# Performance work log

Hardware: AMD Instinct MI355X
Metric: run time of the kernel (lower is better)

## Reference

```python
import jax, jax.numpy as jnp
import numpy as np

C = 128          # channel_size
H = 2            # num_head
HD = C // H      # per-head dim = 64
SCALE = C ** 0.5 # note: module scales by sqrt(channel_size), not sqrt(head_dim)


def setup_inputs() -> dict:
    key = jax.random.key(0)
    k_x, k_w, k_b = jax.random.split(key, 3)
    x = jax.random.normal(k_x, (8, 64, 256, C), dtype=jnp.float32)
    # nn.Linear(C, 3C): weight [3C, C], bias [3C]; y = x @ W.T + b
    bound = 1.0 / np.sqrt(C)
    W_qkv = jax.random.uniform(k_w, (3 * C, C), dtype=jnp.float32, minval=-bound, maxval=bound)
    b_qkv = jax.random.uniform(k_b, (3 * C,), dtype=jnp.float32, minval=-bound, maxval=bound)
    return {"x": x, "W_qkv": W_qkv, "b_qkv": b_qkv}


def reference(x, W_qkv, b_qkv):
    b, l, g, _ = x.shape
    qkv = jnp.einsum('blgc,dc->blgd', x, W_qkv) + b_qkv        # [b,l,g,3C]
    # rearrange 'b l g (d h c) -> d b l h g c'
    qkv = qkv.reshape(b, l, g, 3, H, HD)
    qkv = jnp.transpose(qkv, (3, 0, 1, 4, 2, 5))               # [3,b,l,h,g,c]
    q, k, v = qkv[0], qkv[1], qkv[2]
    score = jnp.einsum('blhgc,blhkc->blhgk', q, k) / SCALE      # [b,l,h,g,g]
    score = jax.nn.softmax(score, axis=-1)
    out = jnp.einsum('blhgk,blhkc->blhgc', score, v)            # [b,l,h,g,c]
    # rearrange 'b l h g c -> b l g (h c)'
    out = jnp.transpose(out, (0, 1, 3, 2, 4)).reshape(b, l, g, H * HD)
    return out
```

## Files before the change

kernel.cpp:

```cpp
#include <hip/hip_runtime.h>
#include <hip/hip_bf16.h>


typedef __bf16 bf16x8 __attribute__((ext_vector_type(8)));
typedef float  f32x4  __attribute__((ext_vector_type(4)));
typedef float  f32x16 __attribute__((ext_vector_type(16)));

#define MFMA16(a, b, c) __builtin_amdgcn_mfma_f32_16x16x32_bf16((a), (b), (c), 0, 0, 0)
#define MFMA32(a, b, c) __builtin_amdgcn_mfma_f32_32x32x16_bf16((a), (b), (c), 0, 0, 0)

namespace dmsa {

constexpr int G  = 256;
constexpr int C  = 128;
constexpr int HD = 64;
constexpr float QSCALE = 1.4426950408889634f * 0.08838834764831845f;

__device__ __forceinline__ unsigned pack2(float a, float b) {
    union { __hip_bfloat162 h; unsigned u; } c;
    c.h = __float22bfloat162_rn(make_float2(a, b));
    return c.u;
}
__device__ __forceinline__ uint2 pack4(float a, float b, float c, float d) {
    uint2 r; r.x = pack2(a, b); r.y = pack2(c, d); return r;
}
__device__ __forceinline__ uint4 pack8(const float* p) {
    uint4 r;
    r.x = pack2(p[0], p[1]); r.y = pack2(p[2], p[3]);
    r.z = pack2(p[4], p[5]); r.w = pack2(p[6], p[7]);
    return r;
}
__device__ __forceinline__ bf16x8 lds8(const ushort* p) { return *(const bf16x8*)p; }
__device__ __forceinline__ bf16x8 ldg8(const ushort* p) { return *(const bf16x8*)p; }
__device__ __forceinline__ bf16x8 ld8f(const float* __restrict__ p) {
    float t[8];
    *(float4*)t       = *(const float4*)p;
    *(float4*)(t + 4) = *(const float4*)(p + 4);
    union { uint4 u; bf16x8 v; } c;
    c.u = pack8(t);
    return c.v;
}

__global__ void convw(const float* __restrict__ W, ushort* __restrict__ wbf) {
    int t = blockIdx.x * 256 + threadIdx.x;
    float tmp[8];
    const float* p = W + (size_t)t * 8;
    *(float4*)tmp       = *(const float4*)p;
    *(float4*)(tmp + 4) = *(const float4*)(p + 4);
    *(uint4*)(wbf + (size_t)t * 8) = pack8(tmp);
}

__global__ __launch_bounds__(512, 4)
void fused(const float* __restrict__ x, const ushort* __restrict__ wb,
           const float* __restrict__ bias, float* __restrict__ out)
{
    __shared__ ushort kc[G * 72];
    __shared__ ushort vc[HD * 264];

    const int tid = threadIdx.x, wv = tid >> 6, lane = tid & 63;
    const int l16 = lane & 15, quad = lane >> 4;
    const int l32 = lane & 31, hl = lane >> 5;

    const int b  = blockIdx.x;
    const int L  = ((b & 7) << 7) | (b >> 3);
    const int bl = L >> 1, h = L & 1;

    const float*  xr = x  + (size_t)bl * G * C;
    const ushort* Wq = wb + (size_t)(h * HD) * C;
    const ushort* Wk = wb + (size_t)(C + h * HD) * C;
    const ushort* Wv = wb + (size_t)(2 * C + h * HD) * C;

    const int r0 = wv * 32;
    const f32x4 z4 = {0.f, 0.f, 0.f, 0.f};

    bf16x8 xf[2][4];
    #pragma unroll
    for (int i = 0; i < 2; ++i)
        #pragma unroll
        for (int kk = 0; kk < 4; ++kk)
            xf[i][kk] = ld8f(xr + (size_t)(r0 + i * 16 + l16) * C + kk * 32 + quad * 8);

    f32x4 qacc[4][2];
    #pragma unroll
    for (int mi = 0; mi < 4; ++mi)
        #pragma unroll
        for (int ni = 0; ni < 2; ++ni) qacc[mi][ni] = z4;
    #pragma unroll
    for (int kk = 0; kk < 4; ++kk)
        #pragma unroll
        for (int mi = 0; mi < 4; ++mi) {
            bf16x8 a = ldg8(Wq + (size_t)(mi * 16 + l16) * C + kk * 32 + quad * 8);
            #pragma unroll
            for (int ni = 0; ni < 2; ++ni)
                qacc[mi][ni] = MFMA16(a, xf[ni][kk], qacc[mi][ni]);
        }
    ushort* qs = kc + r0 * 72;
    #pragma unroll
    for (int mi = 0; mi < 4; ++mi) {
        float4 bs = *(const float4*)(bias + h * HD + mi * 16 + quad * 4);
        #pragma unroll
        for (int ni = 0; ni < 2; ++ni)
            *(uint2*)(qs + (ni * 16 + l16) * 72 + mi * 16 + quad * 4) =
                pack4((qacc[mi][ni][0] + bs.x) * QSCALE,
                      (qacc[mi][ni][1] + bs.y) * QSCALE,
                      (qacc[mi][ni][2] + bs.z) * QSCALE,
                      (qacc[mi][ni][3] + bs.w) * QSCALE);
    }
    bf16x8 qf[4];
    #pragma unroll
    for (int kk = 0; kk < 4; ++kk)
        qf[kk] = lds8(qs + l32 * 72 + kk * 16 + hl * 8);

    {
        f32x4 kacc[4][2];
        #pragma unroll
        for (int mi = 0; mi < 4; ++mi)
            #pragma unroll
            for (int nt = 0; nt < 2; ++nt) kacc[mi][nt] = z4;
        #pragma unroll
        for (int kk = 0; kk < 4; ++kk)
            #pragma unroll
            for (int mi = 0; mi < 4; ++mi) {
                bf16x8 a = ldg8(Wk + (size_t)(mi * 16 + l16) * C + kk * 32 + quad * 8);
                #pragma unroll
                for (int nt = 0; nt < 2; ++nt)
                    kacc[mi][nt] = MFMA16(a, xf[nt][kk], kacc[mi][nt]);
            }
        #pragma unroll
        for (int mi = 0; mi < 4; ++mi) {
            float4 bs = *(const float4*)(bias + C + h * HD + mi * 16 + quad * 4);
            #pragma unroll
            for (int nt = 0; nt < 2; ++nt)
                *(uint2*)(kc + (r0 + nt * 16 + l16) * 72 + mi * 16 + quad * 4) =
                    pack4(kacc[mi][nt][0] + bs.x, kacc[mi][nt][1] + bs.y,
                          kacc[mi][nt][2] + bs.z, kacc[mi][nt][3] + bs.w);
        }
    }

    {
        f32x4 vacc[2][4];
        #pragma unroll
        for (int mt = 0; mt < 2; ++mt)
            #pragma unroll
            for (int nt = 0; nt < 4; ++nt) vacc[mt][nt] = z4;
        #pragma unroll
        for (int kk = 0; kk < 4; ++kk)
            #pragma unroll
            for (int nt = 0; nt < 4; ++nt) {
                bf16x8 bw = ldg8(Wv + (size_t)(nt * 16 + l16) * C + kk * 32 + quad * 8);
                #pragma unroll
                for (int mt = 0; mt < 2; ++mt)
                    vacc[mt][nt] = MFMA16(xf[mt][kk], bw, vacc[mt][nt]);
            }
        #pragma unroll
        for (int nt = 0; nt < 4; ++nt) {
            float bv = bias[2 * C + h * HD + nt * 16 + l16];
            #pragma unroll
            for (int mt = 0; mt < 2; ++mt)
                *(uint2*)(vc + (nt * 16 + l16) * 264 + r0 + mt * 16 + quad * 4) =
                    pack4(vacc[mt][nt][0] + bv, vacc[mt][nt][1] + bv,
                          vacc[mt][nt][2] + bv, vacc[mt][nt][3] + bv);
        }
    }

    __syncthreads();

    float lacc = 0.f;
    f32x16 oacc[2];
    #pragma unroll
    for (int mt = 0; mt < 2; ++mt)
        #pragma unroll
        for (int r = 0; r < 16; ++r) oacc[mt][r] = 0.f;

    #pragma unroll 2
    for (int sp = 0; sp < 8; ++sp) {
        const int g0 = sp * 32;

        bf16x8 kf[4];
        #pragma unroll
        for (int kk = 0; kk < 4; ++kk)
            kf[kk] = lds8(kc + (g0 + l32) * 72 + kk * 16 + hl * 8);
        bf16x8 vf[2][2];
        #pragma unroll
        for (int mt = 0; mt < 2; ++mt)
            #pragma unroll
            for (int ch = 0; ch < 2; ++ch)
                vf[mt][ch] = lds8(vc + (mt * 32 + l32) * 264 + g0 + ch * 16 + hl * 8);

        f32x16 s;
        #pragma unroll
        for (int r = 0; r < 16; ++r) s[r] = 0.f;
        __builtin_amdgcn_s_setprio(1);
        #pragma unroll
        for (int kk = 0; kk < 4; ++kk)
            s = MFMA32(kf[kk], qf[kk], s);
        __builtin_amdgcn_s_setprio(0);

        float part = 0.f;
        #pragma unroll
        for (int r = 0; r < 16; ++r) {
            float p = exp2f(s[r]);
            s[r] = p;
            part += p;
        }
        lacc += part;

        #pragma unroll
        for (int ch = 0; ch < 2; ++ch) {
            unsigned p0a = pack2(s[8 * ch + 0], s[8 * ch + 1]);
            unsigned p0b = pack2(s[8 * ch + 2], s[8 * ch + 3]);
            unsigned p1a = pack2(s[8 * ch + 4], s[8 * ch + 5]);
            unsigned p1b = pack2(s[8 * ch + 6], s[8 * ch + 7]);
            auto w02 = __builtin_amdgcn_permlane32_swap((int)p0a, (int)p1a, false, false);
            auto w13 = __builtin_amdgcn_permlane32_swap((int)p0b, (int)p1b, false, false);
            union { uint4 u; bf16x8 v; } pf;
            pf.u.x = (unsigned)w02[0]; pf.u.y = (unsigned)w13[0];
            pf.u.z = (unsigned)w02[1]; pf.u.w = (unsigned)w13[1];
            __builtin_amdgcn_s_setprio(1);
            #pragma unroll
            for (int mt = 0; mt < 2; ++mt)
                oacc[mt] = MFMA32(vf[mt][ch], pf.v, oacc[mt]);
            __builtin_amdgcn_s_setprio(0);
        }
    }

    float* og = out + (size_t)bl * G * C + h * HD;
    {
        float l = lacc;
        l += __shfl_xor(l, 32);
        float inv = 1.0f / l;
        int g = r0 + l32;
        #pragma unroll
        for (int mt = 0; mt < 2; ++mt)
            #pragma unroll
            for (int rr = 0; rr < 4; ++rr) {
                float4 st;
                st.x = oacc[mt][4 * rr + 0] * inv;
                st.y = oacc[mt][4 * rr + 1] * inv;
                st.z = oacc[mt][4 * rr + 2] * inv;
                st.w = oacc[mt][4 * rr + 3] * inv;
                *(float4*)(og + (size_t)g * C + mt * 32 + rr * 8 + hl * 4) = st;
            }
    }
}

}

extern "C" void kernel_launch(void* const* d_in, const int* in_sizes, int n_in,
                              void* d_out, int out_size, void* d_ws, size_t ws_size,
                              hipStream_t stream) {
    (void)in_sizes; (void)n_in; (void)out_size;

    if (ws_size < (size_t)384 * 128 * 2) return;

    const float* x    = (const float*)d_in[0];
    const float* W    = (const float*)d_in[1];
    const float* bias = (const float*)d_in[2];
    float* out = (float*)d_out;

    ushort* wbf = (ushort*)d_ws;

    dmsa::convw<<<dim3(24),   dim3(256), 0, stream>>>(W, wbf);
    dmsa::fused<<<dim3(1024), dim3(512), 0, stream>>>(x, wbf, bias, out);
}
```

Measured before the change: 186.8 us.

## Make fused attention persistent over four head tiles with double-buffered K/V

Each block now handles two (b,l) rows across both heads, so 256 blocks replace 1024. Each x row is loaded once and reused for both heads, and the next x load is prefetched during attention. K/V shared-memory buffers are double-buffered so the next head's QKV projection runs while the current head is still in flight, with one barrier per iteration. The projections switch from 16x16 to 32x32 MFMA tiles, and occupancy drops to 2 blocks per CU, which leaves only 256 blocks and risks less latency hiding and fewer blocks than CUs can hold.

```diff
diff --git a/kernel.cpp b/kernel.cpp
--- a/kernel.cpp
+++ b/kernel.cpp
@@ -3,10 +3,8 @@
 
 
 typedef __bf16 bf16x8 __attribute__((ext_vector_type(8)));
-typedef float  f32x4  __attribute__((ext_vector_type(4)));
 typedef float  f32x16 __attribute__((ext_vector_type(16)));
 
-#define MFMA16(a, b, c) __builtin_amdgcn_mfma_f32_16x16x32_bf16((a), (b), (c), 0, 0, 0)
 #define MFMA32(a, b, c) __builtin_amdgcn_mfma_f32_32x32x16_bf16((a), (b), (c), 0, 0, 0)
 
 namespace dmsa {
@@ -32,14 +30,6 @@
 }
 __device__ __forceinline__ bf16x8 lds8(const ushort* p) { return *(const bf16x8*)p; }
 __device__ __forceinline__ bf16x8 ldg8(const ushort* p) { return *(const bf16x8*)p; }
-__device__ __forceinline__ bf16x8 ld8f(const float* __restrict__ p) {
-    float t[8];
-    *(float4*)t       = *(const float4*)p;
-    *(float4*)(t + 4) = *(const float4*)(p + 4);
-    union { uint4 u; bf16x8 v; } c;
-    c.u = pack8(t);
-    return c.v;
-}
 
 __global__ void convw(const float* __restrict__ W, ushort* __restrict__ wbf) {
     int t = blockIdx.x * 256 + threadIdx.x;
@@ -50,186 +40,198 @@
     *(uint4*)(wbf + (size_t)t * 8) = pack8(tmp);
 }
 
-__global__ __launch_bounds__(512, 4)
+__global__ __launch_bounds__(512, 2)
 void fused(const float* __restrict__ x, const ushort* __restrict__ wb,
            const float* __restrict__ bias, float* __restrict__ out)
 {
-    __shared__ ushort kc[G * 72];
-    __shared__ ushort vc[HD * 264];
+    __shared__ ushort kcs[2][G * 72];
+    __shared__ ushort vcs[2][HD * 264];
 
     const int tid = threadIdx.x, wv = tid >> 6, lane = tid & 63;
-    const int l16 = lane & 15, quad = lane >> 4;
     const int l32 = lane & 31, hl = lane >> 5;
-
-    const int b  = blockIdx.x;
-    const int L  = ((b & 7) << 7) | (b >> 3);
-    const int bl = L >> 1, h = L & 1;
-
-    const float*  xr = x  + (size_t)bl * G * C;
-    const ushort* Wq = wb + (size_t)(h * HD) * C;
-    const ushort* Wk = wb + (size_t)(C + h * HD) * C;
-    const ushort* Wv = wb + (size_t)(2 * C + h * HD) * C;
-
     const int r0 = wv * 32;
-    const f32x4 z4 = {0.f, 0.f, 0.f, 0.f};
-
-    bf16x8 xf[2][4];
-    #pragma unroll
-    for (int i = 0; i < 2; ++i)
+    const int b = blockIdx.x;
+
+    float4 xraw[16];
+    auto issue_x = [&](int nbl) {
+        const float* px = x + ((size_t)nbl * G + r0 + l32) * C + hl * 8;
+        #pragma unroll
+        for (int kk = 0; kk < 8; ++kk) {
+            xraw[2 * kk]     = *(const float4*)(px + kk * 16);
+            xraw[2 * kk + 1] = *(const float4*)(px + kk * 16 + 4);
+        }
+    };
+    bf16x8 xf[8];
+    auto cvt_x = [&]() {
+        #pragma unroll
+        for (int kk = 0; kk < 8; ++kk) {
+            union { uint4 u; bf16x8 v; } c;
+            c.u = pack8((const float*)&xraw[2 * kk]);
+            xf[kk] = c.v;
+        }
+    };
+
+    bf16x8 qf[4];
+    auto do_gemm = [&](int h_, ushort* kcb, ushort* vcb) {
+        const ushort* Wq = wb + (size_t)(h_ * HD) * C;
+        const ushort* Wk = wb + (size_t)(C + h_ * HD) * C;
+        const ushort* Wv = wb + (size_t)(2 * C + h_ * HD) * C;
+
+        f32x16 qa[2];
+        #pragma unroll
+        for (int mt = 0; mt < 2; ++mt)
+            #pragma unroll
+            for (int r = 0; r < 16; ++r) qa[mt][r] = 0.f;
+        #pragma unroll
+        for (int kk = 0; kk < 8; ++kk)
+            #pragma unroll
+            for (int mt = 0; mt < 2; ++mt) {
+                bf16x8 a = ldg8(Wq + (size_t)(mt * 32 + l32) * C + kk * 16 + hl * 8);
+                qa[mt] = MFMA32(a, xf[kk], qa[mt]);
+            }
+        ushort* qs = kcb + r0 * 72;
+        #pragma unroll
+        for (int mt = 0; mt < 2; ++mt)
+            #pragma unroll
+            for (int j = 0; j < 4; ++j) {
+                int c0 = mt * 32 + j * 8 + hl * 4;
+                float4 bs = *(const float4*)(bias + h_ * HD + c0);
+                *(uint2*)(qs + l32 * 72 + c0) =
+                    pack4((qa[mt][4 * j + 0] + bs.x) * QSCALE,
+                          (qa[mt][4 * j + 1] + bs.y) * QSCALE,
+                          (qa[mt][4 * j + 2] + bs.z) * QSCALE,
+                          (qa[mt][4 * j + 3] + bs.w) * QSCALE);
+            }
         #pragma unroll
         for (int kk = 0; kk < 4; ++kk)
-            xf[i][kk] = ld8f(xr + (size_t)(r0 + i * 16 + l16) * C + kk * 32 + quad * 8);
-
-    f32x4 qacc[4][2];
-    #pragma unroll
-    for (int mi = 0; mi < 4; ++mi)
-        #pragma unroll
-        for (int ni = 0; ni < 2; ++ni) qacc[mi][ni] = z4;
-    #pragma unroll
-    for (int kk = 0; kk < 4; ++kk)
-        #pragma unroll
-        for (int mi = 0; mi < 4; ++mi) {
-            bf16x8 a = ldg8(Wq + (size_t)(mi * 16 + l16) * C + kk * 32 + quad * 8);
-            #pragma unroll
-            for (int ni = 0; ni < 2; ++ni)
-                qacc[mi][ni] = MFMA16(a, xf[ni][kk], qacc[mi][ni]);
-        }
-    ushort* qs = kc + r0 * 72;
-    #pragma unroll
-    for (int mi = 0; mi < 4; ++mi) {
-        float4 bs = *(const float4*)(bias + h * HD + mi * 16 + quad * 4);
-        #pragma unroll
-        for (int ni = 0; ni < 2; ++ni)
-            *(uint2*)(qs + (ni * 16 + l16) * 72 + mi * 16 + quad * 4) =
-                pack4((qacc[mi][ni][0] + bs.x) * QSCALE,
-                      (qacc[mi][ni][1] + bs.y) * QSCALE,
-                      (qacc[mi][ni][2] + bs.z) * QSCALE,
-                      (qacc[mi][ni][3] + bs.w) * QSCALE);
-    }
-    bf16x8 qf[4];
-    #pragma unroll
-    for (int kk = 0; kk < 4; ++kk)
-        qf[kk] = lds8(qs + l32 * 72 + kk * 16 + hl * 8);
-
-    {
-        f32x4 kacc[4][2];
-        #pragma unroll
-        for (int mi = 0; mi < 4; ++mi)
-            #pragma unroll
-            for (int nt = 0; nt < 2; ++nt) kacc[mi][nt] = z4;
-        #pragma unroll
-        for (int kk = 0; kk < 4; ++kk)
-            #pragma unroll
-            for (int mi = 0; mi < 4; ++mi) {
-                bf16x8 a = ldg8(Wk + (size_t)(mi * 16 + l16) * C + kk * 32 + quad * 8);
-                #pragma unroll
-                for (int nt = 0; nt < 2; ++nt)
-                    kacc[mi][nt] = MFMA16(a, xf[nt][kk], kacc[mi][nt]);
-            }
-        #pragma unroll
-        for (int mi = 0; mi < 4; ++mi) {
-            float4 bs = *(const float4*)(bias + C + h * HD + mi * 16 + quad * 4);
-            #pragma unroll
-            for (int nt = 0; nt < 2; ++nt)
-                *(uint2*)(kc + (r0 + nt * 16 + l16) * 72 + mi * 16 + quad * 4) =
-                    pack4(kacc[mi][nt][0] + bs.x, kacc[mi][nt][1] + bs.y,
-                          kacc[mi][nt][2] + bs.z, kacc[mi][nt][3] + bs.w);
-        }
-    }
-
-    {
-        f32x4 vacc[2][4];
-        #pragma unroll
-        for (int mt = 0; mt < 2; ++mt)
-            #pragma unroll
-            for (int nt = 0; nt < 4; ++nt) vacc[mt][nt] = z4;
-        #pragma unroll
-        for (int kk = 0; kk < 4; ++kk)
-            #pragma unroll
-            for (int nt = 0; nt < 4; ++nt) {
-                bf16x8 bw = ldg8(Wv + (size_t)(nt * 16 + l16) * C + kk * 32 + quad * 8);
-                #pragma unroll
-                for (int mt = 0; mt < 2; ++mt)
-                    vacc[mt][nt] = MFMA16(xf[mt][kk], bw, vacc[mt][nt]);
-            }
-        #pragma unroll
-        for (int nt = 0; nt < 4; ++nt) {
-            float bv = bias[2 * C + h * HD + nt * 16 + l16];
-            #pragma unroll
-            for (int mt = 0; mt < 2; ++mt)
-                *(uint2*)(vc + (nt * 16 + l16) * 264 + r0 + mt * 16 + quad * 4) =
-                    pack4(vacc[mt][nt][0] + bv, vacc[mt][nt][1] + bv,
-                          vacc[mt][nt][2] + bv, vacc[mt][nt][3] + bv);
-        }
-    }
-
+            qf[kk] = lds8(qs + l32 * 72 + kk * 16 + hl * 8);
+
+        f32x16 ka[2];
+        #pragma unroll
+        for (int mt = 0; mt < 2; ++mt)
+            #pragma unroll
+            for (int r = 0; r < 16; ++r) ka[mt][r] = 0.f;
+        #pragma unroll
+        for (int kk = 0; kk < 8; ++kk)
+            #pragma unroll
+            for (int mt = 0; mt < 2; ++mt) {
+                bf16x8 a = ldg8(Wk + (size_t)(mt * 32 + l32) * C + kk * 16 + hl * 8);
+                ka[mt] = MFMA32(a, xf[kk], ka[mt]);
+            }
+        #pragma unroll
+        for (int mt = 0; mt < 2; ++mt)
+            #pragma unroll
+            for (int j = 0; j < 4; ++j) {
+                int c0 = mt * 32 + j * 8 + hl * 4;
+                float4 bs = *(const float4*)(bias + C + h_ * HD + c0);
+                *(uint2*)(kcb + (r0 + l32) * 72 + c0) =
+                    pack4(ka[mt][4 * j + 0] + bs.x, ka[mt][4 * j + 1] + bs.y,
+                          ka[mt][4 * j + 2] + bs.z, ka[mt][4 * j + 3] + bs.w);
+            }
+
+        f32x16 va[2];
+        #pragma unroll
+        for (int nt = 0; nt < 2; ++nt)
+            #pragma unroll
+            for (int r = 0; r < 16; ++r) va[nt][r] = 0.f;
+        #pragma unroll
+        for (int kk = 0; kk < 8; ++kk)
+            #pragma unroll
+            for (int nt = 0; nt < 2; ++nt) {
+                bf16x8 bw = ldg8(Wv + (size_t)(nt * 32 + l32) * C + kk * 16 + hl * 8);
+                va[nt] = MFMA32(xf[kk], bw, va[nt]);
+            }
+        #pragma unroll
+        for (int nt = 0; nt < 2; ++nt) {
+            float bv = bias[2 * C + h_ * HD + nt * 32 + l32];
+            #pragma unroll
+            for (int j = 0; j < 4; ++j) {
+                int t0 = j * 8 + hl * 4;
+                *(uint2*)(vcb + (nt * 32 + l32) * 264 + r0 + t0) =
+                    pack4(va[nt][4 * j + 0] + bv, va[nt][4 * j + 1] + bv,
+                          va[nt][4 * j + 2] + bv, va[nt][4 * j + 3] + bv);
+            }
+        }
+    };
+
+    issue_x(2 * b);
+    cvt_x();
+    do_gemm(0, kcs[0], vcs[0]);
     __syncthreads();
 
-    float lacc = 0.f;
-    f32x16 oacc[2];
-    #pragma unroll
-    for (int mt = 0; mt < 2; ++mt)
-        #pragma unroll
-        for (int r = 0; r < 16; ++r) oacc[mt][r] = 0.f;
-
-    #pragma unroll 2
-    for (int sp = 0; sp < 8; ++sp) {
-        const int g0 = sp * 32;
-
-        bf16x8 kf[4];
-        #pragma unroll
-        for (int kk = 0; kk < 4; ++kk)
-            kf[kk] = lds8(kc + (g0 + l32) * 72 + kk * 16 + hl * 8);
-        bf16x8 vf[2][2];
-        #pragma unroll
-        for (int mt = 0; mt < 2; ++mt)
-            #pragma unroll
-            for (int ch = 0; ch < 2; ++ch)
-                vf[mt][ch] = lds8(vc + (mt * 32 + l32) * 264 + g0 + ch * 16 + hl * 8);
-
-        f32x16 s;
-        #pragma unroll
-        for (int r = 0; r < 16; ++r) s[r] = 0.f;
-        __builtin_amdgcn_s_setprio(1);
-        #pragma unroll
-        for (int kk = 0; kk < 4; ++kk)
-            s = MFMA32(kf[kk], qf[kk], s);
-        __builtin_amdgcn_s_setprio(0);
-
-        float part = 0.f;
-        #pragma unroll
-        for (int r = 0; r < 16; ++r) {
-            float p = exp2f(s[r]);
-            s[r] = p;
-            part += p;
-        }
-        lacc += part;
-
-        #pragma unroll
-        for (int ch = 0; ch < 2; ++ch) {
-            unsigned p0a = pack2(s[8 * ch + 0], s[8 * ch + 1]);
-            unsigned p0b = pack2(s[8 * ch + 2], s[8 * ch + 3]);
-            unsigned p1a = pack2(s[8 * ch + 4], s[8 * ch + 5]);
-            unsigned p1b = pack2(s[8 * ch + 6], s[8 * ch + 7]);
-            auto w02 = __builtin_amdgcn_permlane32_swap((int)p0a, (int)p1a, false, false);
-            auto w13 = __builtin_amdgcn_permlane32_swap((int)p0b, (int)p1b, false, false);
-            union { uint4 u; bf16x8 v; } pf;
-            pf.u.x = (unsigned)w02[0]; pf.u.y = (unsigned)w13[0];
-            pf.u.z = (unsigned)w02[1]; pf.u.w = (unsigned)w13[1];
-            __builtin_amdgcn_s_setprio(1);
-            #pragma unroll
-            for (int mt = 0; mt < 2; ++mt)
-                oacc[mt] = MFMA32(vf[mt][ch], pf.v, oacc[mt]);
-            __builtin_amdgcn_s_setprio(0);
-        }
-    }
-
-    float* og = out + (size_t)bl * G * C + h * HD;
-    {
-        float l = lacc;
-        l += __shfl_xor(l, 32);
+    #pragma unroll 1
+    for (int it = 0; it < 4; ++it) {
+        const int L = 4 * b + it, bl = L >> 1, h = L & 1, cur = it & 1;
+        ushort* kcb = kcs[cur];
+        ushort* vcb = vcs[cur];
+
+        f32x16 oacc[2];
+        #pragma unroll
+        for (int mt = 0; mt < 2; ++mt)
+            #pragma unroll
+            for (int r = 0; r < 16; ++r) oacc[mt][r] = 0.f;
+        float lacc = 0.f;
+
+        #pragma unroll
+        for (int sp = 0; sp < 4; ++sp) {
+            if (it == 1 && sp == 3) issue_x(2 * b + 1);
+
+            bf16x8 kf[2][4];
+            #pragma unroll
+            for (int mi = 0; mi < 2; ++mi)
+                #pragma unroll
+                for (int kk = 0; kk < 4; ++kk)
+                    kf[mi][kk] = lds8(kcb + (sp * 64 + mi * 32 + l32) * 72
+                                      + kk * 16 + hl * 8);
+
+            f32x16 s[2];
+            #pragma unroll
+            for (int mi = 0; mi < 2; ++mi)
+                #pragma unroll
+                for (int r = 0; r < 16; ++r) s[mi][r] = 0.f;
+            #pragma unroll
+            for (int kk = 0; kk < 4; ++kk)
+                #pragma unroll
+                for (int mi = 0; mi < 2; ++mi)
+                    s[mi] = MFMA32(kf[mi][kk], qf[kk], s[mi]);
+
+            float part = 0.f;
+            #pragma unroll
+            for (int mi = 0; mi < 2; ++mi)
+                #pragma unroll
+                for (int r = 0; r < 16; ++r) {
+                    float p = exp2f(s[mi][r]);
+                    s[mi][r] = p;
+                    part += p;
+                }
+            lacc += part;
+
+            #pragma unroll
+            for (int mi = 0; mi < 2; ++mi)
+                #pragma unroll
+                for (int ch = 0; ch < 2; ++ch) {
+                    unsigned p0a = pack2(s[mi][8 * ch + 0], s[mi][8 * ch + 1]);
+                    unsigned p0b = pack2(s[mi][8 * ch + 2], s[mi][8 * ch + 3]);
+                    unsigned p1a = pack2(s[mi][8 * ch + 4], s[mi][8 * ch + 5]);
+                    unsigned p1b = pack2(s[mi][8 * ch + 6], s[mi][8 * ch + 7]);
+                    auto w02 = __builtin_amdgcn_permlane32_swap((int)p0a, (int)p1a, false, false);
+                    auto w13 = __builtin_amdgcn_permlane32_swap((int)p0b, (int)p1b, false, false);
+                    union { uint4 u; bf16x8 v; } pf;
+                    pf.u.x = (unsigned)w02[0]; pf.u.y = (unsigned)w13[0];
+                    pf.u.z = (unsigned)w02[1]; pf.u.w = (unsigned)w13[1];
+                    const int cc = 2 * mi + ch;
+                    #pragma unroll
+                    for (int mt = 0; mt < 2; ++mt) {
+                        bf16x8 vf = lds8(vcb + (mt * 32 + l32) * 264
+                                         + sp * 64 + cc * 16 + hl * 8);
+                        oacc[mt] = MFMA32(vf, pf.v, oacc[mt]);
+                    }
+                }
+        }
+
+        float l = lacc + __shfl_xor(lacc, 32);
         float inv = 1.0f / l;
-        int g = r0 + l32;
+        float* og = out + (size_t)bl * G * C + h * HD + (size_t)(r0 + l32) * C;
         #pragma unroll
         for (int mt = 0; mt < 2; ++mt)
             #pragma unroll
@@ -239,8 +241,14 @@
                 st.y = oacc[mt][4 * rr + 1] * inv;
                 st.z = oacc[mt][4 * rr + 2] * inv;
                 st.w = oacc[mt][4 * rr + 3] * inv;
-                *(float4*)(og + (size_t)g * C + mt * 32 + rr * 8 + hl * 4) = st;
-            }
+                *(float4*)(og + mt * 32 + rr * 8 + hl * 4) = st;
+            }
+
+        if (it < 3) {
+            if (it == 1) cvt_x();
+            do_gemm((it + 1) & 1, kcs[cur ^ 1], vcs[cur ^ 1]);
+        }
+        __syncthreads();
     }
 }
 
@@ -260,6 +268,6 @@
 
     ushort* wbf = (ushort*)d_ws;
 
-    dmsa::convw<<<dim3(24),   dim3(256), 0, stream>>>(W, wbf);
-    dmsa::fused<<<dim3(1024), dim3(512), 0, stream>>>(x, wbf, bias, out);
-}
+    dmsa::convw<<<dim3(24),  dim3(256), 0, stream>>>(W, wbf);
+    dmsa::fused<<<dim3(256), dim3(512), 0, stream>>>(x, wbf, bias, out);
+}
```

After: 237.2 us. +27.0%, slower.
